# Kernel tuning notes

Hardware: AMD Instinct MI355X
Metric: run time of the kernel (lower is better)

Reference implementation:

```python
import jax, jax.numpy as jnp
import numpy as np

WSIZES = (4, 8, 16)
IDX = (0, 1, 2, 1, 2, 0, 2, 0, 1)
BN_EPS = 1e-5


def _window_qv(el, ws):
    # el: [B, 2c, H, W] -> q, v each [(B*h*w), ws*ws, c]
    # matches rearrange 'b (qv c) (h dh) (w dw) -> qv (b h w) (dh dw) c'
    B, C2, H, W = el.shape
    c = C2 // 2
    h, w = H // ws, W // ws
    t = el.reshape(B, 2, c, h, ws, w, ws)
    t = t.transpose(1, 0, 3, 5, 4, 6, 2)  # qv, B, h, w, dh, dw, c
    t = t.reshape(2, B * h * w, ws * ws, c)
    return t[0], t[1]


def _match_batch(t, target_b):
    # replicate torch reshape-based window expansion/contraction
    b, s, c = t.shape
    if b < target_b:  # 'b (c wsize) h -> (b wsize) c h'
        ws = target_b // b
        return t.reshape(b, s // ws, ws, c).transpose(0, 2, 1, 3).reshape(b * ws, s // ws, c)
    if b > target_b:  # '(b wsize) c h -> b (c wsize) h'
        ws = b // target_b
        return t.reshape(target_b, ws, s, c).transpose(0, 2, 1, 3).reshape(target_b, s * ws, c)
    return t


def _unwindow(t, B, H, W, ws):
    # '(b h w) (dh dw) c -> b c (h dh) (w dw)'
    h, w = H // ws, W // ws
    c = t.shape[-1]
    return t.reshape(B, h, w, ws, ws, c).transpose(0, 5, 1, 3, 2, 4).reshape(B, c, H, W)


def _gmsa(x, w_in, b_in, bn_gamma, bn_beta, bn_mean, bn_var, w_out, b_out):
    B, C, H, W = x.shape
    # 1x1 conv + BatchNorm (eval-mode affine normalization)
    y = jnp.einsum('bchw,oc->bohw', x, w_in) + b_in[None, :, None, None]
    inv = bn_gamma / jnp.sqrt(bn_var + BN_EPS)
    y = y * inv[None, :, None, None] + (bn_beta - bn_mean * inv)[None, :, None, None]

    split = C * 2 // 3
    qs, vs = [], []
    for i, ws in enumerate(WSIZES):
        el = y[:, i * split:(i + 1) * split]
        el = jnp.roll(el, (-(ws // 2), -(ws // 2)), axis=(2, 3))  # shifts > 0
        q, v = _window_qv(el, ws)
        qs.append(q)
        vs.append(v)

    outs = []
    for i in range(0, 9, 3):
        q = qs[IDX[i]]
        k = _match_batch(qs[IDX[i + 1]], q.shape[0])
        v = _match_batch(vs[IDX[i + 2]], q.shape[0])
        atn = jax.nn.softmax(jnp.einsum('bic,bjc->bij', q, k), axis=-1)
        outs.append(jnp.einsum('bij,bjc->bic', atn, v))

    ys = []
    for i, ws in enumerate(WSIZES):
        yb = _unwindow(outs[i], B, H, W, ws)
        yb = jnp.roll(yb, (ws // 2, ws // 2), axis=(2, 3))
        ys.append(yb)
    y = jnp.concatenate(ys, axis=1)
    return jnp.einsum('bchw,oc->bohw', y, w_out) + b_out[None, :, None, None]


def setup_inputs() -> dict:
    key = jax.random.key(0)
    ks = jax.random.split(key, 9)
    C = 96
    return {
        'x': jax.random.normal(ks[0], (8, C, 256, 256), dtype=jnp.float32),
        'w_in': jax.random.normal(ks[1], (2 * C, C), dtype=jnp.float32) * (1.0 / np.sqrt(C)),
        'b_in': jax.random.normal(ks[2], (2 * C,), dtype=jnp.float32) * 0.02,
        'bn_gamma': jax.random.uniform(ks[3], (2 * C,), dtype=jnp.float32, minval=0.5, maxval=1.5),
        'bn_beta': jax.random.normal(ks[4], (2 * C,), dtype=jnp.float32) * 0.02,
        'bn_mean': jax.random.normal(ks[5], (2 * C,), dtype=jnp.float32) * 0.1,
        'bn_var': jax.random.uniform(ks[6], (2 * C,), dtype=jnp.float32, minval=0.5, maxval=1.5),
        'w_out': jax.random.normal(ks[7], (C, C), dtype=jnp.float32) * (1.0 / np.sqrt(C)),
        'b_out': jax.random.normal(ks[8], (C,), dtype=jnp.float32) * 0.02,
    }


def reference(x, w_in, b_in, bn_gamma, bn_beta, bn_mean, bn_var, w_out, b_out):
    return _gmsa(x, w_in, b_in, bn_gamma, bn_beta, bn_mean, bn_var, w_out, b_out)
```

## Files before the change

kernel.cpp:

```cpp
#include <hip/hip_runtime.h>


typedef _Float16 f16x8 __attribute__((ext_vector_type(8)));
typedef _Float16 f16x4 __attribute__((ext_vector_type(4)));
typedef _Float16 f16x2 __attribute__((ext_vector_type(2)));
typedef float    f32x4 __attribute__((ext_vector_type(4)));

__device__ inline float exp2_fast(float x) {
    float r; asm("v_exp_f32 %0, %1" : "=v"(r) : "v"(x)); return r;
}
__device__ inline unsigned pkrtz(float a, float b) {
    return __builtin_bit_cast(unsigned, __builtin_amdgcn_cvt_pkrtz(a, b));
}

__global__ __launch_bounds__(256) void k_prep(
    const float* __restrict__ w_in, const float* __restrict__ b_in,
    const float* __restrict__ gma, const float* __restrict__ bta,
    const float* __restrict__ mu,  const float* __restrict__ var,
    const float* __restrict__ w_out,
    _Float16* __restrict__ wf, float* __restrict__ bs, _Float16* __restrict__ wo)
{
    const int t = threadIdx.x;
    if (t < 192) {
        const float qs = ((t & 63) < 32) ? 1.2011224087864498f : 1.0f;
        float iv = gma[t] * rsqrtf(var[t] + 1e-5f);
        float s  = iv * qs;
        bs[t] = (b_in[t]*iv + bta[t] - mu[t]*iv) * qs;
        #pragma unroll
        for (int c4 = 0; c4 < 96; c4 += 4) {
            float4 w = *reinterpret_cast<const float4*>(w_in + t*96 + c4);
            f16x4 h;
            h[0]=(_Float16)(w.x*s); h[1]=(_Float16)(w.y*s);
            h[2]=(_Float16)(w.z*s); h[3]=(_Float16)(w.w*s);
            *reinterpret_cast<f16x4*>(wf + t*96 + c4) = h;
        }
    }
    if (t < 96) {
        #pragma unroll
        for (int c4 = 0; c4 < 96; c4 += 4) {
            float4 w = *reinterpret_cast<const float4*>(w_out + t*96 + c4);
            f16x4 h;
            h[0]=(_Float16)w.x; h[1]=(_Float16)w.y;
            h[2]=(_Float16)w.z; h[3]=(_Float16)w.w;
            *reinterpret_cast<f16x4*>(wo + t*96 + c4) = h;
        }
    }
}

__global__ __launch_bounds__(256) void k_conv_in(
    const float* __restrict__ x, const _Float16* __restrict__ wf,
    const float* __restrict__ bs,
    _Float16* __restrict__ q0, _Float16* __restrict__ v0,
    _Float16* __restrict__ q1, _Float16* __restrict__ v1,
    _Float16* __restrict__ q2, _Float16* __restrict__ v2)
{
    __shared__ unsigned xs2[2][16*132];
    const int t  = threadIdx.x;
    const int wv = t >> 6, ln = t & 63;
    const int lo = ln & 15, hi = ln >> 4;
    const int oh = wv >> 1, ph = wv & 1;

    const int pixbase = blockIdx.x * 128;
    const int b   = pixbase >> 16;
    const int rem = pixbase & 65535;
    const int hh  = rem >> 8;
    const int ww0 = rem & 255;

    const int r0 = t >> 5;
    const int q4 = (t & 31) << 2;
    const float* xb = x + (size_t)b*96*65536 + rem + q4;

    float4 L0, L1, L2, L3;

#define CLOAD(c0) { \
    L0 = *reinterpret_cast<const float4*>(xb + (size_t)(c0 + 2*r0     )*65536); \
    L1 = *reinterpret_cast<const float4*>(xb + (size_t)(c0 + 2*r0 +  1)*65536); \
    L2 = *reinterpret_cast<const float4*>(xb + (size_t)(c0 + 2*r0 + 16)*65536); \
    L3 = *reinterpret_cast<const float4*>(xb + (size_t)(c0 + 2*r0 + 17)*65536); }
#define CWRITE(bf) { \
    uint4 u0, u1; \
    u0.x = pkrtz(L0.x, L1.x); u0.y = pkrtz(L0.y, L1.y); \
    u0.z = pkrtz(L0.z, L1.z); u0.w = pkrtz(L0.w, L1.w); \
    u1.x = pkrtz(L2.x, L3.x); u1.y = pkrtz(L2.y, L3.y); \
    u1.z = pkrtz(L2.z, L3.z); u1.w = pkrtz(L2.w, L3.w); \
    *reinterpret_cast<uint4*>(&xs2[bf][ r0     *132 + q4]) = u0; \
    *reinterpret_cast<uint4*>(&xs2[bf][(r0 + 8)*132 + q4]) = u1; }
#define CCOMP(bf, ks) { \
    _Pragma("unroll") for (int cf = 0; cf < 4; ++cf) { \
        const unsigned* bp = &xs2[bf][hi*4*132 + ph*64 + cf*16 + lo]; \
        uint4 u; u.x = bp[0]; u.y = bp[132]; u.z = bp[264]; u.w = bp[396]; \
        f16x8 bfv = __builtin_bit_cast(f16x8, u); \
        _Pragma("unroll") for (int rf = 0; rf < 6; ++rf) \
            acc[rf][cf] = __builtin_amdgcn_mfma_f32_16x16x32_f16( \
                              af[rf][ks], bfv, acc[rf][cf], 0,0,0); } }

    CLOAD(0);

    f16x8 af[6][3];
    const _Float16* wrow0 = wf + (size_t)(oh*96 + lo)*96 + hi*8;
    #pragma unroll
    for (int rf = 0; rf < 6; ++rf)
        #pragma unroll
        for (int ks = 0; ks < 3; ++ks)
            af[rf][ks] = *reinterpret_cast<const f16x8*>(wrow0 + rf*16*96 + ks*32);

    f32x4 acc[6][4];
    #pragma unroll
    for (int rf = 0; rf < 6; ++rf)
        #pragma unroll
        for (int cf = 0; cf < 4; ++cf) acc[rf][cf] = f32x4{0.f,0.f,0.f,0.f};

    CWRITE(0);
    __syncthreads();
    CLOAD(32);
    CCOMP(0, 0);
    CWRITE(1);
    __syncthreads();
    CLOAD(64);
    CCOMP(1, 1);
    CWRITE(0);
    __syncthreads();
    CCOMP(0, 2);

    int ro[3][4];
    #pragma unroll
    for (int i = 0; i < 3; ++i) {
        const int lg = 2 + i;
        const int ws = 1 << lg;
        const int sft = ws >> 1;
        const int nblk = 256 >> lg;
        int h  = (hh - sft) & 255;
        int nbrow = (b*nblk + (h >> lg))*nblk;
        int hr = h & (ws-1);
        #pragma unroll
        for (int cf = 0; cf < 4; ++cf) {
            int w = (ww0 + ph*64 + cf*16 + lo - sft) & 255;
            ro[i][cf] = (nbrow + (w >> lg))*(ws*ws) + hr*ws + (w & (ws-1));
        }
    }
    #pragma unroll
    for (int rf = 0; rf < 6; ++rf) {
        const int base = oh*96 + rf*16;
        const int o0i  = base + hi*4;
        const int sc   = base >> 6;
        const bool isv = (base & 32) != 0;
        const int c32  = o0i & 31;
        float4 bi = *reinterpret_cast<const float4*>(bs + o0i);
        _Float16* tb = (sc == 0) ? (isv ? v0 : q0)
                     : (sc == 1) ? (isv ? v1 : q1)
                                 : (isv ? v2 : q2);
        #pragma unroll
        for (int cf = 0; cf < 4; ++cf) {
            f16x4 hv;
            hv[0] = (_Float16)(acc[rf][cf][0] + bi.x);
            hv[1] = (_Float16)(acc[rf][cf][1] + bi.y);
            hv[2] = (_Float16)(acc[rf][cf][2] + bi.z);
            hv[3] = (_Float16)(acc[rf][cf][3] + bi.w);
            *reinterpret_cast<f16x4*>(tb + (size_t)ro[sc][cf]*32 + c32) = hv;
        }
    }
#undef CLOAD
#undef CWRITE
#undef CCOMP
}

template<int GROUP>
__device__ __forceinline__ void attn_body(
    int bid, uint4* Kl, _Float16* Vt, _Float16* Pl,
    const _Float16* __restrict__ Q, const _Float16* __restrict__ Ks,
    const _Float16* Vs, _Float16* O)
{
    constexpr int S   = (GROUP==0) ? 16 : (GROUP==1) ? 64 : 256;
    constexpr int GB  = 256 / S;
    constexpr int KT  = (S < 32) ? 16 : 32;
    constexpr int NT  = S / KT;
    constexpr int CBS = KT / 16;

    const int t = threadIdx.x;
    {
        const int g = t / S, j = t % S;
        const int bq = bid * GB + g;
        int krow, vrow;
        if constexpr (GROUP == 0) {
            krow = (bq >> 2)*64  + (j << 2) + (bq & 3);
            vrow = (bq >> 4)*256 + (j << 4) + (bq & 15);
        } else if constexpr (GROUP == 1) {
            krow = (bq >> 2)*256 + (j << 2) + (bq & 3);
            vrow = ((bq << 2) + (j & 3))*16 + (j >> 2);
        } else {
            krow = ((bq << 4) + (j & 15))*16 + (j >> 4);
            vrow = ((bq << 2) + (j & 3))*64 + (j >> 2);
        }
        const uint4* ks = reinterpret_cast<const uint4*>(Ks + (size_t)krow*32);
        uint4 ka = ks[0], kb = ks[1], kc = ks[2], kd = ks[3];
        Kl[0*256 + t] = ka; Kl[1*256 + t] = kb;
        Kl[2*256 + t] = kc; Kl[3*256 + t] = kd;
        union { uint4 u4[4]; _Float16 h[32]; } vb;
        const uint4* vs = reinterpret_cast<const uint4*>(Vs + (size_t)vrow*32);
        vb.u4[0] = vs[0]; vb.u4[1] = vs[1]; vb.u4[2] = vs[2]; vb.u4[3] = vs[3];
        #pragma unroll
        for (int d = 0; d < 32; ++d) Vt[d*264 + t] = vb.h[d];
        Vt[(t >> 3)*264 + 256 + (t & 7)] = (_Float16)0.f;
        if (t < 8) Vt[32*264 + t] = (_Float16)0.f;
    }
    const int wv = t >> 6, ln = t & 63;
    const int lo = ln & 15, hi = ln >> 4;
    _Float16* Pw = Pl + wv*(64*40);
    if constexpr (S == 16) {
        uint* pw32 = reinterpret_cast<uint*>(Pw);
        #pragma unroll
        for (int k2 = 0; k2 < 8; ++k2) {
            int idx = ln + k2*64;
            pw32[(idx >> 3)*20 + 8 + (idx & 7)] = 0u;
        }
    }
    __syncthreads();

    const int rowbase = bid*256 + wv*64;
    f16x8 qf[4];
    #pragma unroll
    for (int rb = 0; rb < 4; ++rb) {
        uint4 qv = *reinterpret_cast<const uint4*>(
            Q + ((size_t)(rowbase + rb*16 + lo))*32 + hi*8);
        qf[rb] = __builtin_bit_cast(f16x8, qv);
    }

    f32x4 ofr[4][2];
    float m[4], ls[4];
    #pragma unroll
    for (int rb = 0; rb < 4; ++rb) {
        m[rb] = -1e30f; ls[rb] = 0.f;
        ofr[rb][0] = f32x4{0.f,0.f,0.f,0.f};
        ofr[rb][1] = f32x4{0.f,0.f,0.f,0.f};
    }
    const f32x4 zf = f32x4{0.f,0.f,0.f,0.f};

    for (int tt = 0; tt < NT; ++tt) {
        f32x4 sf[4][CBS];
        if constexpr (S == 16) {
            #pragma unroll
            for (int rb = 0; rb < 4; ++rb) {
                int key = wv*64 + rb*16 + lo;
                f16x8 bk = __builtin_bit_cast(f16x8, Kl[hi*256 + key]);
                sf[rb][0] = __builtin_amdgcn_mfma_f32_16x16x32_f16(bk, qf[rb], zf, 0,0,0);
            }
        } else {
            f16x8 bk[CBS];
            const int wb = (S == 64) ? wv*64 : 0;
            #pragma unroll
            for (int cb = 0; cb < CBS; ++cb) {
                int key = wb + tt*KT + cb*16 + lo;
                bk[cb] = __builtin_bit_cast(f16x8, Kl[hi*256 + key]);
            }
            #pragma unroll
            for (int rb = 0; rb < 4; ++rb)
                #pragma unroll
                for (int cb = 0; cb < CBS; ++cb)
                    sf[rb][cb] = __builtin_amdgcn_mfma_f32_16x16x32_f16(bk[cb], qf[rb], zf, 0,0,0);
        }

        #pragma unroll
        for (int rb = 0; rb < 4; ++rb) {
            float tm = sf[rb][0][0];
            #pragma unroll
            for (int cb = 0; cb < CBS; ++cb)
                #pragma unroll
                for (int r = 0; r < 4; ++r)
                    if (cb | r) tm = fmaxf(tm, sf[rb][cb][r]);
            tm = fmaxf(tm, __shfl_xor(tm, 16));
            tm = fmaxf(tm, __shfl_xor(tm, 32));
            float mn = fmaxf(m[rb], tm);
            float sc = exp2_fast(m[rb] - mn);
            m[rb] = mn;
            float ps = 0.f;
            #pragma unroll
            for (int cb = 0; cb < CBS; ++cb) {
                float p0 = exp2_fast(sf[rb][cb][0] - mn);
                float p1 = exp2_fast(sf[rb][cb][1] - mn);
                float p2 = exp2_fast(sf[rb][cb][2] - mn);
                float p3 = exp2_fast(sf[rb][cb][3] - mn);
                ps += (p0+p1)+(p2+p3);
                unsigned w01 = pkrtz(p0, p1);
                unsigned w23 = pkrtz(p2, p3);
                _Float16* pp = Pw + (rb*16 + lo)*40 + cb*16 + hi*4;
                *reinterpret_cast<unsigned*>(pp)     = w01;
                *reinterpret_cast<unsigned*>(pp + 2) = w23;
            }
            ls[rb] = ls[rb]*sc + ps;
            float s0 = __shfl(sc, hi*4 + 0);
            float s1 = __shfl(sc, hi*4 + 1);
            float s2 = __shfl(sc, hi*4 + 2);
            float s3 = __shfl(sc, hi*4 + 3);
            ofr[rb][0][0]*=s0; ofr[rb][0][1]*=s1; ofr[rb][0][2]*=s2; ofr[rb][0][3]*=s3;
            ofr[rb][1][0]*=s0; ofr[rb][1][1]*=s1; ofr[rb][1][2]*=s2; ofr[rb][1][3]*=s3;
        }

        #pragma unroll
        for (int rb = 0; rb < 4; ++rb) {
            f16x8 pa = *reinterpret_cast<const f16x8*>(Pw + (rb*16 + lo)*40 + hi*8);
            const int wb = (S == 16) ? wv*64 + rb*16 : (S == 64) ? wv*64 : 0;
            const int key0 = wb + tt*KT + hi*8;
            #pragma unroll
            for (int dcb = 0; dcb < 2; ++dcb) {
                f16x8 bv = *reinterpret_cast<const f16x8*>(Vt + (dcb*16 + lo)*264 + key0);
                ofr[rb][dcb] = __builtin_amdgcn_mfma_f32_16x16x32_f16(pa, bv, ofr[rb][dcb], 0,0,0);
            }
        }
    }

    #pragma unroll
    for (int rb = 0; rb < 4; ++rb) {
        float v = ls[rb];
        v += __shfl_xor(v, 16);
        v += __shfl_xor(v, 32);
        float linv = 1.f / v;
        float l0 = __shfl(linv, hi*4 + 0);
        float l1 = __shfl(linv, hi*4 + 1);
        float l2 = __shfl(linv, hi*4 + 2);
        float l3 = __shfl(linv, hi*4 + 3);
        #pragma unroll
        for (int dcb = 0; dcb < 2; ++dcb) {
            float lr[4] = {l0, l1, l2, l3};
            #pragma unroll
            for (int r = 0; r < 4; ++r) {
                float ov = ofr[rb][dcb][r] * lr[r];
                int row = rowbase + rb*16 + hi*4 + r;
                O[(size_t)row*32 + dcb*16 + lo] = (_Float16)ov;
            }
        }
    }
}

__global__ __launch_bounds__(256) void k_attn_all(
    const _Float16* __restrict__ q0, const _Float16* __restrict__ v0,
    const _Float16* __restrict__ q1, const _Float16* __restrict__ v1,
    const _Float16* __restrict__ q2, const _Float16* __restrict__ v2)
{
    __shared__ __align__(16) char smem[16384 + 16912 + 20480];
    uint4*    Kl = reinterpret_cast<uint4*>(smem);
    _Float16* Vt = reinterpret_cast<_Float16*>(smem + 16384);
    _Float16* Pl = reinterpret_cast<_Float16*>(smem + 16384 + 16912);
    const int bid = (int)blockIdx.x;
    if (bid < 2048)
        attn_body<0>(bid, Kl, Vt, Pl, q0, q1, v2, const_cast<_Float16*>(v2));
    else if (bid < 4096)
        attn_body<1>(bid - 2048, Kl, Vt, Pl, q1, q2, v0, const_cast<_Float16*>(v0));
    else
        attn_body<2>(bid - 4096, Kl, Vt, Pl, q2, q0, v1, const_cast<_Float16*>(v1));
}

__global__ __launch_bounds__(256) void k_conv_out(
    const _Float16* __restrict__ o0, const _Float16* __restrict__ o1,
    const _Float16* __restrict__ o2, const _Float16* __restrict__ wo,
    const float* __restrict__ b_out, float* __restrict__ out)
{
    constexpr int YS = 104;
    __shared__ _Float16 yt[256*YS];
    const int t  = threadIdx.x;
    const int wv = t >> 6, ln = t & 63;
    const int lo = ln & 15, hi = ln >> 4;
    const int bid = (int)blockIdx.x;
    const int swz = (bid & 7)*256 + (bid >> 3);
    const int b = swz >> 8;
    const int h = swz & 255;

    #pragma unroll
    for (int i = 0; i < 3; ++i) {
        const int lg = 2 + i;
        const int ws = 1 << lg;
        const int sft = ws >> 1;
        const int nblk = 256 >> lg;
        int hh = (h - sft) & 255;
        int w  = (t - sft) & 255;
        int nb = (b*nblk + (hh >> lg))*nblk + (w >> lg);
        int roff = nb*(ws*ws) + (hh & (ws-1))*ws + (w & (ws-1));
        const uint4* src = reinterpret_cast<const uint4*>(
            (i==0 ? o0 : i==1 ? o1 : o2) + (size_t)roff*32);
        uint4 r0 = src[0], r1 = src[1], r2 = src[2], r3 = src[3];
        uint4* dst = reinterpret_cast<uint4*>(&yt[t*YS + i*32]);
        dst[0] = r0; dst[1] = r1; dst[2] = r2; dst[3] = r3;
    }

    f16x8 af[6][3];
    #pragma unroll
    for (int rf = 0; rf < 6; ++rf)
        #pragma unroll
        for (int ks = 0; ks < 3; ++ks)
            af[rf][ks] = *reinterpret_cast<const f16x8*>(
                wo + (rf*16 + lo)*96 + ks*32 + hi*8);
    __syncthreads();

    f32x4 acc[6][4];
    #pragma unroll
    for (int rf = 0; rf < 6; ++rf)
        #pragma unroll
        for (int cf = 0; cf < 4; ++cf) acc[rf][cf] = f32x4{0.f,0.f,0.f,0.f};

    #pragma unroll
    for (int cf = 0; cf < 4; ++cf) {
        const int px = wv*64 + cf*16 + lo;
        #pragma unroll
        for (int ks = 0; ks < 3; ++ks) {
            f16x8 bfv = *reinterpret_cast<const f16x8*>(&yt[px*YS + ks*32 + hi*8]);
            #pragma unroll
            for (int rf = 0; rf < 6; ++rf)
                acc[rf][cf] = __builtin_amdgcn_mfma_f32_16x16x32_f16(
                                  af[rf][ks], bfv, acc[rf][cf], 0,0,0);
        }
    }

    const size_t obase = (size_t)b*96*65536 + (size_t)h*256;
    #pragma unroll
    for (int rf = 0; rf < 6; ++rf) {
        const int oo = rf*16 + hi*4;
        float4 bi = *reinterpret_cast<const float4*>(b_out + oo);
        #pragma unroll
        for (int cf = 0; cf < 4; ++cf) {
            const int px = wv*64 + cf*16 + lo;
            out[obase + (size_t)(oo+0)*65536 + px] = acc[rf][cf][0] + bi.x;
            out[obase + (size_t)(oo+1)*65536 + px] = acc[rf][cf][1] + bi.y;
            out[obase + (size_t)(oo+2)*65536 + px] = acc[rf][cf][2] + bi.z;
            out[obase + (size_t)(oo+3)*65536 + px] = acc[rf][cf][3] + bi.w;
        }
    }
}

extern "C" void kernel_launch(void* const* d_in, const int* in_sizes, int n_in,
                              void* d_out, int out_size, void* d_ws, size_t ws_size,
                              hipStream_t stream)
{
    const float* x     = (const float*)d_in[0];
    const float* w_in  = (const float*)d_in[1];
    const float* b_in  = (const float*)d_in[2];
    const float* gma   = (const float*)d_in[3];
    const float* bta   = (const float*)d_in[4];
    const float* mu    = (const float*)d_in[5];
    const float* var   = (const float*)d_in[6];
    const float* w_out = (const float*)d_in[7];
    const float* b_out = (const float*)d_in[8];
    float* out = (float*)d_out;

    _Float16* W = (_Float16*)d_ws;
    const size_t M = 16777216;
    _Float16 *q0 = W,       *v0 = W +   M, *q1 = W + 2*M,
             *v1 = W + 3*M, *q2 = W + 4*M, *v2 = W + 5*M;
    _Float16* wf = W + 6*M;
    float*    bs = (float*)(W + 6*M + 18432);
    _Float16* wo = W + 6*M + 18432 + 384;

    k_prep<<<1, 256, 0, stream>>>(w_in, b_in, gma, bta, mu, var, w_out, wf, bs, wo);
    k_conv_in<<<4096, 256, 0, stream>>>(x, wf, bs, q0, v0, q1, v1, q2, v2);
    k_attn_all<<<6144, 256, 0, stream>>>(q0, v0, q1, v1, q2, v2);
    k_conv_out<<<2048, 256, 0, stream>>>(v2, v0, v1, wo, b_out, out);
}
```

Baseline: 276.8 us.

## Replace online softmax with full-row softmax in attention; deepen conv_in prefetch

The attention kernel drops the tiled online-softmax loop. For each 16-query row block it computes all score fragments at once, takes one max and exponentiates once, and stages P in a repacked shared-memory layout. This removes the per-tile rescale shuffles and multiplies. The input conv kernel uses a third LDS buffer and issues the second channel-chunk load before the first compute, so more global loads are in flight. The cost is higher register pressure for the S=256 group, which holds 16 score fragments live.

```diff
diff --git a/kernel.cpp b/kernel.cpp
--- a/kernel.cpp
+++ b/kernel.cpp
@@ -3,7 +3,6 @@
 
 typedef _Float16 f16x8 __attribute__((ext_vector_type(8)));
 typedef _Float16 f16x4 __attribute__((ext_vector_type(4)));
-typedef _Float16 f16x2 __attribute__((ext_vector_type(2)));
 typedef float    f32x4 __attribute__((ext_vector_type(4)));
 
 __device__ inline float exp2_fast(float x) {
@@ -54,7 +53,7 @@
     _Float16* __restrict__ q1, _Float16* __restrict__ v1,
     _Float16* __restrict__ q2, _Float16* __restrict__ v2)
 {
-    __shared__ unsigned xs2[2][16*132];
+    __shared__ unsigned xs2[3][16*132];
     const int t  = threadIdx.x;
     const int wv = t >> 6, ln = t & 63;
     const int lo = ln & 15, hi = ln >> 4;
@@ -70,31 +69,32 @@
     const int q4 = (t & 31) << 2;
     const float* xb = x + (size_t)b*96*65536 + rem + q4;
 
-    float4 L0, L1, L2, L3;
-
-#define CLOAD(c0) { \
-    L0 = *reinterpret_cast<const float4*>(xb + (size_t)(c0 + 2*r0     )*65536); \
-    L1 = *reinterpret_cast<const float4*>(xb + (size_t)(c0 + 2*r0 +  1)*65536); \
-    L2 = *reinterpret_cast<const float4*>(xb + (size_t)(c0 + 2*r0 + 16)*65536); \
-    L3 = *reinterpret_cast<const float4*>(xb + (size_t)(c0 + 2*r0 + 17)*65536); }
-#define CWRITE(bf) { \
+    float4 A0, A1, A2, A3, B0, B1, B2, B3;
+
+#define CLOAD(Ra,Rb,Rc,Rd,c0) { \
+    Ra = *reinterpret_cast<const float4*>(xb + (size_t)(c0 + 2*r0     )*65536); \
+    Rb = *reinterpret_cast<const float4*>(xb + (size_t)(c0 + 2*r0 +  1)*65536); \
+    Rc = *reinterpret_cast<const float4*>(xb + (size_t)(c0 + 2*r0 + 16)*65536); \
+    Rd = *reinterpret_cast<const float4*>(xb + (size_t)(c0 + 2*r0 + 17)*65536); }
+#define CWRITE(sl,Ra,Rb,Rc,Rd) { \
     uint4 u0, u1; \
-    u0.x = pkrtz(L0.x, L1.x); u0.y = pkrtz(L0.y, L1.y); \
-    u0.z = pkrtz(L0.z, L1.z); u0.w = pkrtz(L0.w, L1.w); \
-    u1.x = pkrtz(L2.x, L3.x); u1.y = pkrtz(L2.y, L3.y); \
-    u1.z = pkrtz(L2.z, L3.z); u1.w = pkrtz(L2.w, L3.w); \
-    *reinterpret_cast<uint4*>(&xs2[bf][ r0     *132 + q4]) = u0; \
-    *reinterpret_cast<uint4*>(&xs2[bf][(r0 + 8)*132 + q4]) = u1; }
-#define CCOMP(bf, ks) { \
+    u0.x = pkrtz(Ra.x, Rb.x); u0.y = pkrtz(Ra.y, Rb.y); \
+    u0.z = pkrtz(Ra.z, Rb.z); u0.w = pkrtz(Ra.w, Rb.w); \
+    u1.x = pkrtz(Rc.x, Rd.x); u1.y = pkrtz(Rc.y, Rd.y); \
+    u1.z = pkrtz(Rc.z, Rd.z); u1.w = pkrtz(Rc.w, Rd.w); \
+    *reinterpret_cast<uint4*>(&xs2[sl][ r0     *132 + q4]) = u0; \
+    *reinterpret_cast<uint4*>(&xs2[sl][(r0 + 8)*132 + q4]) = u1; }
+#define CCOMP(sl, ks) { \
     _Pragma("unroll") for (int cf = 0; cf < 4; ++cf) { \
-        const unsigned* bp = &xs2[bf][hi*4*132 + ph*64 + cf*16 + lo]; \
+        const unsigned* bp = &xs2[sl][hi*4*132 + ph*64 + cf*16 + lo]; \
         uint4 u; u.x = bp[0]; u.y = bp[132]; u.z = bp[264]; u.w = bp[396]; \
         f16x8 bfv = __builtin_bit_cast(f16x8, u); \
         _Pragma("unroll") for (int rf = 0; rf < 6; ++rf) \
             acc[rf][cf] = __builtin_amdgcn_mfma_f32_16x16x32_f16( \
                               af[rf][ks], bfv, acc[rf][cf], 0,0,0); } }
 
-    CLOAD(0);
+    CLOAD(A0, A1, A2, A3, 0);
+    CLOAD(B0, B1, B2, B3, 32);
 
     f16x8 af[6][3];
     const _Float16* wrow0 = wf + (size_t)(oh*96 + lo)*96 + hi*8;
@@ -110,17 +110,16 @@
         #pragma unroll
         for (int cf = 0; cf < 4; ++cf) acc[rf][cf] = f32x4{0.f,0.f,0.f,0.f};
 
-    CWRITE(0);
+    CWRITE(0, A0, A1, A2, A3);
     __syncthreads();
-    CLOAD(32);
+    CLOAD(A0, A1, A2, A3, 64);
     CCOMP(0, 0);
-    CWRITE(1);
+    CWRITE(1, B0, B1, B2, B3);
     __syncthreads();
-    CLOAD(64);
     CCOMP(1, 1);
-    CWRITE(0);
+    CWRITE(2, A0, A1, A2, A3);
     __syncthreads();
-    CCOMP(0, 2);
+    CCOMP(2, 2);
 
     int ro[3][4];
     #pragma unroll
@@ -166,15 +165,17 @@
 
 template<int GROUP>
 __device__ __forceinline__ void attn_body(
-    int bid, uint4* Kl, _Float16* Vt, _Float16* Pl,
+    int bid, uint4* Kl, _Float16* Vt, unsigned* P32,
     const _Float16* __restrict__ Q, const _Float16* __restrict__ Ks,
     const _Float16* Vs, _Float16* O)
 {
     constexpr int S   = (GROUP==0) ? 16 : (GROUP==1) ? 64 : 256;
     constexpr int GB  = 256 / S;
-    constexpr int KT  = (S < 32) ? 16 : 32;
-    constexpr int NT  = S / KT;
-    constexpr int CBS = KT / 16;
+    constexpr int NFR = S / 16;
+    constexpr int NTL = (S == 16) ? 1 : S / 32;
+    constexpr int NH  = (S == 256) ? 2 : 1;
+    constexpr int FH  = NFR / NH;
+    constexpr int TPH = NTL / NH;
 
     const int t = threadIdx.x;
     {
@@ -200,19 +201,13 @@
         vb.u4[0] = vs[0]; vb.u4[1] = vs[1]; vb.u4[2] = vs[2]; vb.u4[3] = vs[3];
         #pragma unroll
         for (int d = 0; d < 32; ++d) Vt[d*264 + t] = vb.h[d];
-        Vt[(t >> 3)*264 + 256 + (t & 7)] = (_Float16)0.f;
-        if (t < 8) Vt[32*264 + t] = (_Float16)0.f;
     }
     const int wv = t >> 6, ln = t & 63;
     const int lo = ln & 15, hi = ln >> 4;
-    _Float16* Pw = Pl + wv*(64*40);
+    unsigned* Pw = P32 + wv*1056;
     if constexpr (S == 16) {
-        uint* pw32 = reinterpret_cast<uint*>(Pw);
-        #pragma unroll
-        for (int k2 = 0; k2 < 8; ++k2) {
-            int idx = ln + k2*64;
-            pw32[(idx >> 3)*20 + 8 + (idx & 7)] = 0u;
-        }
+        uint2 z; z.x = 0u; z.y = 0u;
+        *reinterpret_cast<uint2*>(Pw + (ln >> 2)*66 + 8 + (ln & 3)*2) = z;
     }
     __syncthreads();
 
@@ -224,93 +219,58 @@
             Q + ((size_t)(rowbase + rb*16 + lo))*32 + hi*8);
         qf[rb] = __builtin_bit_cast(f16x8, qv);
     }
-
-    f32x4 ofr[4][2];
-    float m[4], ls[4];
+    const f32x4 zf = f32x4{0.f,0.f,0.f,0.f};
+
     #pragma unroll
     for (int rb = 0; rb < 4; ++rb) {
-        m[rb] = -1e30f; ls[rb] = 0.f;
-        ofr[rb][0] = f32x4{0.f,0.f,0.f,0.f};
-        ofr[rb][1] = f32x4{0.f,0.f,0.f,0.f};
-    }
-    const f32x4 zf = f32x4{0.f,0.f,0.f,0.f};
-
-    for (int tt = 0; tt < NT; ++tt) {
-        f32x4 sf[4][CBS];
-        if constexpr (S == 16) {
+        const int KBr = (S == 16) ? wv*64 + rb*16 : (S == 64) ? wv*64 : 0;
+        f32x4 sf[NFR];
+        #pragma unroll
+        for (int f = 0; f < NFR; ++f) {
+            const int key = KBr + f*16 + lo;
+            f16x8 bk = __builtin_bit_cast(f16x8, Kl[hi*256 + key]);
+            sf[f] = __builtin_amdgcn_mfma_f32_16x16x32_f16(bk, qf[rb], zf, 0,0,0);
+        }
+        float m0 = sf[0][0], m1 = sf[0][1], m2 = sf[0][2], m3 = sf[0][3];
+        #pragma unroll
+        for (int f = 1; f < NFR; ++f) {
+            m0 = fmaxf(m0, sf[f][0]); m1 = fmaxf(m1, sf[f][1]);
+            m2 = fmaxf(m2, sf[f][2]); m3 = fmaxf(m3, sf[f][3]);
+        }
+        float mx = fmaxf(fmaxf(m0, m1), fmaxf(m2, m3));
+        mx = fmaxf(mx, __shfl_xor(mx, 16));
+        mx = fmaxf(mx, __shfl_xor(mx, 32));
+
+        float ls0 = 0.f, ls1 = 0.f, ls2 = 0.f, ls3 = 0.f;
+        f32x4 ofr0 = zf, ofr1 = zf;
+        #pragma unroll
+        for (int h = 0; h < NH; ++h) {
             #pragma unroll
-            for (int rb = 0; rb < 4; ++rb) {
-                int key = wv*64 + rb*16 + lo;
-                f16x8 bk = __builtin_bit_cast(f16x8, Kl[hi*256 + key]);
-                sf[rb][0] = __builtin_amdgcn_mfma_f32_16x16x32_f16(bk, qf[rb], zf, 0,0,0);
-            }
-        } else {
-            f16x8 bk[CBS];
-            const int wb = (S == 64) ? wv*64 : 0;
-            #pragma unroll
-            for (int cb = 0; cb < CBS; ++cb) {
-                int key = wb + tt*KT + cb*16 + lo;
-                bk[cb] = __builtin_bit_cast(f16x8, Kl[hi*256 + key]);
+            for (int fl = 0; fl < FH; ++fl) {
+                const int f = h*FH + fl;
+                float p0 = exp2_fast(sf[f][0] - mx);
+                float p1 = exp2_fast(sf[f][1] - mx);
+                float p2 = exp2_fast(sf[f][2] - mx);
+                float p3 = exp2_fast(sf[f][3] - mx);
+                ls0 += p0; ls1 += p1; ls2 += p2; ls3 += p3;
+                uint2 w; w.x = pkrtz(p0, p1); w.y = pkrtz(p2, p3);
+                *reinterpret_cast<uint2*>(Pw + lo*66 + fl*8 + hi*2) = w;
             }
             #pragma unroll
-            for (int rb = 0; rb < 4; ++rb)
-                #pragma unroll
-                for (int cb = 0; cb < CBS; ++cb)
-                    sf[rb][cb] = __builtin_amdgcn_mfma_f32_16x16x32_f16(bk[cb], qf[rb], zf, 0,0,0);
-        }
-
-        #pragma unroll
-        for (int rb = 0; rb < 4; ++rb) {
-            float tm = sf[rb][0][0];
-            #pragma unroll
-            for (int cb = 0; cb < CBS; ++cb)
-                #pragma unroll
-                for (int r = 0; r < 4; ++r)
-                    if (cb | r) tm = fmaxf(tm, sf[rb][cb][r]);
-            tm = fmaxf(tm, __shfl_xor(tm, 16));
-            tm = fmaxf(tm, __shfl_xor(tm, 32));
-            float mn = fmaxf(m[rb], tm);
-            float sc = exp2_fast(m[rb] - mn);
-            m[rb] = mn;
-            float ps = 0.f;
-            #pragma unroll
-            for (int cb = 0; cb < CBS; ++cb) {
-                float p0 = exp2_fast(sf[rb][cb][0] - mn);
-                float p1 = exp2_fast(sf[rb][cb][1] - mn);
-                float p2 = exp2_fast(sf[rb][cb][2] - mn);
-                float p3 = exp2_fast(sf[rb][cb][3] - mn);
-                ps += (p0+p1)+(p2+p3);
-                unsigned w01 = pkrtz(p0, p1);
-                unsigned w23 = pkrtz(p2, p3);
-                _Float16* pp = Pw + (rb*16 + lo)*40 + cb*16 + hi*4;
-                *reinterpret_cast<unsigned*>(pp)     = w01;
-                *reinterpret_cast<unsigned*>(pp + 2) = w23;
+            for (int tl = 0; tl < TPH; ++tl) {
+                const unsigned* pp = Pw + lo*66 + tl*16 + hi*4;
+                uint2 a  = *reinterpret_cast<const uint2*>(pp);
+                uint2 b2 = *reinterpret_cast<const uint2*>(pp + 2);
+                uint4 pu; pu.x = a.x; pu.y = a.y; pu.z = b2.x; pu.w = b2.y;
+                f16x8 pa = __builtin_bit_cast(f16x8, pu);
+                const int key0 = (KBr + (h*TPH + tl)*32 + hi*8) & 255;
+                f16x8 bv0 = *reinterpret_cast<const f16x8*>(Vt + (     lo)*264 + key0);
+                ofr0 = __builtin_amdgcn_mfma_f32_16x16x32_f16(pa, bv0, ofr0, 0,0,0);
+                f16x8 bv1 = *reinterpret_cast<const f16x8*>(Vt + (16 + lo)*264 + key0);
+                ofr1 = __builtin_amdgcn_mfma_f32_16x16x32_f16(pa, bv1, ofr1, 0,0,0);
             }
-            ls[rb] = ls[rb]*sc + ps;
-            float s0 = __shfl(sc, hi*4 + 0);
-            float s1 = __shfl(sc, hi*4 + 1);
-            float s2 = __shfl(sc, hi*4 + 2);
-            float s3 = __shfl(sc, hi*4 + 3);
-            ofr[rb][0][0]*=s0; ofr[rb][0][1]*=s1; ofr[rb][0][2]*=s2; ofr[rb][0][3]*=s3;
-            ofr[rb][1][0]*=s0; ofr[rb][1][1]*=s1; ofr[rb][1][2]*=s2; ofr[rb][1][3]*=s3;
-        }
-
-        #pragma unroll
-        for (int rb = 0; rb < 4; ++rb) {
-            f16x8 pa = *reinterpret_cast<const f16x8*>(Pw + (rb*16 + lo)*40 + hi*8);
-            const int wb = (S == 16) ? wv*64 + rb*16 : (S == 64) ? wv*64 : 0;
-            const int key0 = wb + tt*KT + hi*8;
-            #pragma unroll
-            for (int dcb = 0; dcb < 2; ++dcb) {
-                f16x8 bv = *reinterpret_cast<const f16x8*>(Vt + (dcb*16 + lo)*264 + key0);
-                ofr[rb][dcb] = __builtin_amdgcn_mfma_f32_16x16x32_f16(pa, bv, ofr[rb][dcb], 0,0,0);
-            }
-        }
-    }
-
-    #pragma unroll
-    for (int rb = 0; rb < 4; ++rb) {
-        float v = ls[rb];
+        }
+        float v = (ls0 + ls1) + (ls2 + ls3);
         v += __shfl_xor(v, 16);
         v += __shfl_xor(v, 32);
         float linv = 1.f / v;
@@ -318,16 +278,15 @@
         float l1 = __shfl(linv, hi*4 + 1);
         float l2 = __shfl(linv, hi*4 + 2);
         float l3 = __shfl(linv, hi*4 + 3);
-        #pragma unroll
-        for (int dcb = 0; dcb < 2; ++dcb) {
-            float lr[4] = {l0, l1, l2, l3};
-            #pragma unroll
-            for (int r = 0; r < 4; ++r) {
-                float ov = ofr[rb][dcb][r] * lr[r];
-                int row = rowbase + rb*16 + hi*4 + r;
-                O[(size_t)row*32 + dcb*16 + lo] = (_Float16)ov;
-            }
-        }
+        const int rowb = rowbase + rb*16 + hi*4;
+        O[(size_t)(rowb+0)*32      + lo] = (_Float16)(ofr0[0] * l0);
+        O[(size_t)(rowb+1)*32      + lo] = (_Float16)(ofr0[1] * l1);
+        O[(size_t)(rowb+2)*32      + lo] = (_Float16)(ofr0[2] * l2);
+        O[(size_t)(rowb+3)*32      + lo] = (_Float16)(ofr0[3] * l3);
+        O[(size_t)(rowb+0)*32 + 16 + lo] = (_Float16)(ofr1[0] * l0);
+        O[(size_t)(rowb+1)*32 + 16 + lo] = (_Float16)(ofr1[1] * l1);
+        O[(size_t)(rowb+2)*32 + 16 + lo] = (_Float16)(ofr1[2] * l2);
+        O[(size_t)(rowb+3)*32 + 16 + lo] = (_Float16)(ofr1[3] * l3);
     }
 }
 
@@ -336,17 +295,17 @@
     const _Float16* __restrict__ q1, const _Float16* __restrict__ v1,
     const _Float16* __restrict__ q2, const _Float16* __restrict__ v2)
 {
-    __shared__ __align__(16) char smem[16384 + 16912 + 20480];
-    uint4*    Kl = reinterpret_cast<uint4*>(smem);
-    _Float16* Vt = reinterpret_cast<_Float16*>(smem + 16384);
-    _Float16* Pl = reinterpret_cast<_Float16*>(smem + 16384 + 16912);
+    __shared__ __align__(16) char smem[16384 + 16896 + 16896];
+    uint4*    Kl  = reinterpret_cast<uint4*>(smem);
+    _Float16* Vt  = reinterpret_cast<_Float16*>(smem + 16384);
+    unsigned* P32 = reinterpret_cast<unsigned*>(smem + 16384 + 16896);
     const int bid = (int)blockIdx.x;
     if (bid < 2048)
-        attn_body<0>(bid, Kl, Vt, Pl, q0, q1, v2, const_cast<_Float16*>(v2));
+        attn_body<0>(bid, Kl, Vt, P32, q0, q1, v2, const_cast<_Float16*>(v2));
     else if (bid < 4096)
-        attn_body<1>(bid - 2048, Kl, Vt, Pl, q1, q2, v0, const_cast<_Float16*>(v0));
+        attn_body<1>(bid - 2048, Kl, Vt, P32, q1, q2, v0, const_cast<_Float16*>(v0));
     else
-        attn_body<2>(bid - 4096, Kl, Vt, Pl, q2, q0, v1, const_cast<_Float16*>(v1));
+        attn_body<2>(bid - 4096, Kl, Vt, P32, q2, q0, v1, const_cast<_Float16*>(v1));
 }
 
 __global__ __launch_bounds__(256) void k_conv_out(
```

New measurement: 348.5 us. 25.9% more time.

## Process four pixel tiles per block in conv_in with a continuous load pipeline

Applied to the files above, without the earlier changes.

Each conv_in block now handles four consecutive 128-pixel tiles, 512 pixels in total, and launches a quarter as many blocks. Global loads for the x chunks are prefetched two stages ahead through a triple-buffered LDS ring. This lets loads for the next tile overlap compute and stores of the current one and amortizes the weight-fragment loads. The cost is fewer blocks, which may reduce occupancy and latency hiding, plus more register pressure from two staged load sets.

```diff
diff --git a/kernel.cpp b/kernel.cpp
--- a/kernel.cpp
+++ b/kernel.cpp
@@ -3,7 +3,6 @@
 
 typedef _Float16 f16x8 __attribute__((ext_vector_type(8)));
 typedef _Float16 f16x4 __attribute__((ext_vector_type(4)));
-typedef _Float16 f16x2 __attribute__((ext_vector_type(2)));
 typedef float    f32x4 __attribute__((ext_vector_type(4)));
 
 __device__ inline float exp2_fast(float x) {
@@ -54,47 +53,47 @@
     _Float16* __restrict__ q1, _Float16* __restrict__ v1,
     _Float16* __restrict__ q2, _Float16* __restrict__ v2)
 {
-    __shared__ unsigned xs2[2][16*132];
+    __shared__ unsigned xs2[3][16*132];
     const int t  = threadIdx.x;
     const int wv = t >> 6, ln = t & 63;
     const int lo = ln & 15, hi = ln >> 4;
     const int oh = wv >> 1, ph = wv & 1;
 
-    const int pixbase = blockIdx.x * 128;
-    const int b   = pixbase >> 16;
-    const int rem = pixbase & 65535;
-    const int hh  = rem >> 8;
-    const int ww0 = rem & 255;
+    const int base_px = blockIdx.x * 512;
+    const int b    = base_px >> 16;
+    const int rem0 = base_px & 65535;
 
     const int r0 = t >> 5;
     const int q4 = (t & 31) << 2;
-    const float* xb = x + (size_t)b*96*65536 + rem + q4;
-
-    float4 L0, L1, L2, L3;
-
-#define CLOAD(c0) { \
-    L0 = *reinterpret_cast<const float4*>(xb + (size_t)(c0 + 2*r0     )*65536); \
-    L1 = *reinterpret_cast<const float4*>(xb + (size_t)(c0 + 2*r0 +  1)*65536); \
-    L2 = *reinterpret_cast<const float4*>(xb + (size_t)(c0 + 2*r0 + 16)*65536); \
-    L3 = *reinterpret_cast<const float4*>(xb + (size_t)(c0 + 2*r0 + 17)*65536); }
-#define CWRITE(bf) { \
+    const float* xbb = x + (size_t)b*96*65536 + rem0 + q4;
+
+    float4 RS[2][4];
+
+#define CLOAD(st, cch) { \
+    const float* xp_ = xbb + ((cch)/3)*128 + (size_t)(((cch)%3)*32 + 2*r0)*65536; \
+    RS[st][0] = *reinterpret_cast<const float4*>(xp_); \
+    RS[st][1] = *reinterpret_cast<const float4*>(xp_ + (size_t)   65536); \
+    RS[st][2] = *reinterpret_cast<const float4*>(xp_ + (size_t)16*65536); \
+    RS[st][3] = *reinterpret_cast<const float4*>(xp_ + (size_t)17*65536); }
+#define CWRITE(sl, st) { \
     uint4 u0, u1; \
-    u0.x = pkrtz(L0.x, L1.x); u0.y = pkrtz(L0.y, L1.y); \
-    u0.z = pkrtz(L0.z, L1.z); u0.w = pkrtz(L0.w, L1.w); \
-    u1.x = pkrtz(L2.x, L3.x); u1.y = pkrtz(L2.y, L3.y); \
-    u1.z = pkrtz(L2.z, L3.z); u1.w = pkrtz(L2.w, L3.w); \
-    *reinterpret_cast<uint4*>(&xs2[bf][ r0     *132 + q4]) = u0; \
-    *reinterpret_cast<uint4*>(&xs2[bf][(r0 + 8)*132 + q4]) = u1; }
-#define CCOMP(bf, ks) { \
+    u0.x = pkrtz(RS[st][0].x, RS[st][1].x); u0.y = pkrtz(RS[st][0].y, RS[st][1].y); \
+    u0.z = pkrtz(RS[st][0].z, RS[st][1].z); u0.w = pkrtz(RS[st][0].w, RS[st][1].w); \
+    u1.x = pkrtz(RS[st][2].x, RS[st][3].x); u1.y = pkrtz(RS[st][2].y, RS[st][3].y); \
+    u1.z = pkrtz(RS[st][2].z, RS[st][3].z); u1.w = pkrtz(RS[st][2].w, RS[st][3].w); \
+    *reinterpret_cast<uint4*>(&xs2[sl][ r0     *132 + q4]) = u0; \
+    *reinterpret_cast<uint4*>(&xs2[sl][(r0 + 8)*132 + q4]) = u1; }
+#define CCOMP(sl, ks) { \
     _Pragma("unroll") for (int cf = 0; cf < 4; ++cf) { \
-        const unsigned* bp = &xs2[bf][hi*4*132 + ph*64 + cf*16 + lo]; \
+        const unsigned* bp = &xs2[sl][hi*4*132 + ph*64 + cf*16 + lo]; \
         uint4 u; u.x = bp[0]; u.y = bp[132]; u.z = bp[264]; u.w = bp[396]; \
         f16x8 bfv = __builtin_bit_cast(f16x8, u); \
         _Pragma("unroll") for (int rf = 0; rf < 6; ++rf) \
             acc[rf][cf] = __builtin_amdgcn_mfma_f32_16x16x32_f16( \
                               af[rf][ks], bfv, acc[rf][cf], 0,0,0); } }
 
-    CLOAD(0);
+    CLOAD(0, 0);
+    CLOAD(1, 1);
 
     f16x8 af[6][3];
     const _Float16* wrow0 = wf + (size_t)(oh*96 + lo)*96 + hi*8;
@@ -110,54 +109,59 @@
         #pragma unroll
         for (int cf = 0; cf < 4; ++cf) acc[rf][cf] = f32x4{0.f,0.f,0.f,0.f};
 
-    CWRITE(0);
+    CWRITE(0, 0);
     __syncthreads();
-    CLOAD(32);
-    CCOMP(0, 0);
-    CWRITE(1);
-    __syncthreads();
-    CLOAD(64);
-    CCOMP(1, 1);
-    CWRITE(0);
-    __syncthreads();
-    CCOMP(0, 2);
-
-    int ro[3][4];
-    #pragma unroll
-    for (int i = 0; i < 3; ++i) {
-        const int lg = 2 + i;
-        const int ws = 1 << lg;
-        const int sft = ws >> 1;
-        const int nblk = 256 >> lg;
-        int h  = (hh - sft) & 255;
-        int nbrow = (b*nblk + (h >> lg))*nblk;
-        int hr = h & (ws-1);
-        #pragma unroll
-        for (int cf = 0; cf < 4; ++cf) {
-            int w = (ww0 + ph*64 + cf*16 + lo - sft) & 255;
-            ro[i][cf] = (nbrow + (w >> lg))*(ws*ws) + hr*ws + (w & (ws-1));
-        }
-    }
-    #pragma unroll
-    for (int rf = 0; rf < 6; ++rf) {
-        const int base = oh*96 + rf*16;
-        const int o0i  = base + hi*4;
-        const int sc   = base >> 6;
-        const bool isv = (base & 32) != 0;
-        const int c32  = o0i & 31;
-        float4 bi = *reinterpret_cast<const float4*>(bs + o0i);
-        _Float16* tb = (sc == 0) ? (isv ? v0 : q0)
-                     : (sc == 1) ? (isv ? v1 : q1)
-                                 : (isv ? v2 : q2);
-        #pragma unroll
-        for (int cf = 0; cf < 4; ++cf) {
-            f16x4 hv;
-            hv[0] = (_Float16)(acc[rf][cf][0] + bi.x);
-            hv[1] = (_Float16)(acc[rf][cf][1] + bi.y);
-            hv[2] = (_Float16)(acc[rf][cf][2] + bi.z);
-            hv[3] = (_Float16)(acc[rf][cf][3] + bi.w);
-            *reinterpret_cast<f16x4*>(tb + (size_t)ro[sc][cf]*32 + c32) = hv;
-        }
+
+    #pragma unroll
+    for (int c = 0; c < 12; ++c) {
+        CCOMP(c % 3, c % 3);
+        if ((c % 3) == 2) {
+            const int T   = c / 3;
+            const int rem = rem0 + T*128;
+            const int hh  = rem >> 8;
+            const int ww0 = rem & 255;
+            int ro[3][4];
+            #pragma unroll
+            for (int i = 0; i < 3; ++i) {
+                const int lg = 2 + i;
+                const int ws = 1 << lg;
+                const int sft = ws >> 1;
+                const int nblk = 256 >> lg;
+                int h  = (hh - sft) & 255;
+                int nbrow = (b*nblk + (h >> lg))*nblk;
+                int hr = h & (ws-1);
+                #pragma unroll
+                for (int cf = 0; cf < 4; ++cf) {
+                    int w = (ww0 + ph*64 + cf*16 + lo - sft) & 255;
+                    ro[i][cf] = (nbrow + (w >> lg))*(ws*ws) + hr*ws + (w & (ws-1));
+                }
+            }
+            #pragma unroll
+            for (int rf = 0; rf < 6; ++rf) {
+                const int base = oh*96 + rf*16;
+                const int o0i  = base + hi*4;
+                const int sc   = base >> 6;
+                const bool isv = (base & 32) != 0;
+                const int c32  = o0i & 31;
+                float4 bi = *reinterpret_cast<const float4*>(bs + o0i);
+                _Float16* tb = (sc == 0) ? (isv ? v0 : q0)
+                             : (sc == 1) ? (isv ? v1 : q1)
+                                         : (isv ? v2 : q2);
+                #pragma unroll
+                for (int cf = 0; cf < 4; ++cf) {
+                    f16x4 hv;
+                    hv[0] = (_Float16)(acc[rf][cf][0] + bi.x);
+                    hv[1] = (_Float16)(acc[rf][cf][1] + bi.y);
+                    hv[2] = (_Float16)(acc[rf][cf][2] + bi.z);
+                    hv[3] = (_Float16)(acc[rf][cf][3] + bi.w);
+                    *reinterpret_cast<f16x4*>(tb + (size_t)ro[sc][cf]*32 + c32) = hv;
+                    acc[rf][cf] = f32x4{0.f,0.f,0.f,0.f};
+                }
+            }
+        }
+        if (c + 1 < 12) CWRITE((c + 1) % 3, (c + 1) & 1);
+        if (c + 2 < 12) CLOAD(c & 1, c + 2);
+        __syncthreads();
     }
 #undef CLOAD
 #undef CWRITE
@@ -449,7 +453,7 @@
     _Float16* wo = W + 6*M + 18432 + 384;
 
     k_prep<<<1, 256, 0, stream>>>(w_in, b_in, gma, bta, mu, var, w_out, wf, bs, wo);
-    k_conv_in<<<4096, 256, 0, stream>>>(x, wf, bs, q0, v0, q1, v1, q2, v2);
+    k_conv_in<<<1024, 256, 0, stream>>>(x, wf, bs, q0, v0, q1, v1, q2, v2);
     k_attn_all<<<6144, 256, 0, stream>>>(q0, v0, q1, v1, q2, v2);
     k_conv_out<<<2048, 256, 0, stream>>>(v2, v0, v1, wo, b_out, out);
 }
```

Measured after the change: 290.5 us. 4.9% more time.
